# Kernel optimization log

Hardware: AMD Instinct MI355X
Metric: run time of the kernel (lower is better)

The kernel has to match this reference:

```python
import jax, jax.numpy as jnp
import numpy as np

B, S, NGB, NG, DIM = 64, 4096, 13, 48, 3
NCH = [8, 8, 1]
NSHELLS = 8


def setup_inputs() -> dict:
    key = jax.random.key(0)
    ks = jax.random.split(key, 16)
    rng = np.random.default_rng(0)
    # valid row-wise permutations of the N_ngb neighbor slots per group op
    GnnPerms = jnp.asarray(np.argsort(rng.random((NG, NGB)), axis=1), dtype=jnp.int64)
    NNSites = jax.random.randint(ks[0], (NGB, S), 0, S, dtype=jnp.int64)
    SitesToShells = jax.random.randint(ks[1], (S,), 0, NSHELLS, dtype=jnp.int64)
    # block-diagonal (Ng*dim, Ng*dim) cartesian rotation blocks
    blk = rng.normal(size=(NG, DIM, DIM)).astype(np.float32) * 0.5
    gd = np.zeros((NG * DIM, NG * DIM), np.float32)
    for g in range(NG):
        gd[g * DIM:(g + 1) * DIM, g * DIM:(g + 1) * DIM] = blk[g]
    gdiags = jnp.asarray(gd)
    std = 0.2
    return {
        "InStates": jax.random.normal(ks[2], (B, 1, S), jnp.float32),
        "Psi0": jax.random.normal(ks[3], (NCH[0], 1, NGB), jnp.float32) * std,
        "bias0": jax.random.normal(ks[4], (NCH[0], 1), jnp.float32) * std,
        "Psi1": jax.random.normal(ks[5], (NCH[1], NCH[0], NGB), jnp.float32) * std,
        "bias1": jax.random.normal(ks[6], (NCH[1], 1), jnp.float32) * std,
        "Psi2": jax.random.normal(ks[7], (NCH[2], NCH[1], NGB), jnp.float32) * std,
        "bias2": jax.random.normal(ks[8], (NCH[2], 1), jnp.float32) * std,
        "wtVC": jax.random.normal(ks[9], (DIM, NGB), jnp.float32) * std,
        "ShellWeights": jax.random.normal(ks[10], (NSHELLS,), jnp.float32) * std,
        "gdiags": gdiags,
        "GnnPerms": GnnPerms,
        "NNSites": NNSites,
        "SitesToShells": SitesToShells,
    }


def _rearrange(x, NNSites):
    # x: (B, Nch, S) -> (B, Nch*N_ngb, S); subchannel j of channel c holds x[b, c, NNSites[j, s]]
    b, c, s = x.shape
    return x[:, :, NNSites].reshape(b, c * NGB, s)


def _gconv(x, W, b):
    # x: (B, NchIn*N_ngb, S); W: (NchOut, NchIn, N_ngb); b: (NchOut, 1)
    # group-rotated weights: GW[o, g, c*N_ngb+j] = W[o, c, GnnPerms[g, j]]
    GW = _gconv.GW_cache  # set per-call below via closure-free pattern; replaced in reference
    raise NotImplementedError


def reference(InStates, Psi0, bias0, Psi1, bias1, Psi2, bias2, wtVC,
              ShellWeights, gdiags, GnnPerms, NNSites, SitesToShells):
    act = jax.nn.softplus

    def gconv(x, W, b):
        # rotated weights: (NchOut, Ng, NchIn*N_ngb)
        GW = W[:, :, GnnPerms].transpose(0, 2, 1, 3).reshape(W.shape[0], NG, -1)
        h = jnp.einsum('ogk,bks->bogs', GW, x) + b[:, :, None]  # (B, NchOut, Ng, S)
        return act(h).mean(axis=2)                               # group-orbit average

    out = _rearrange(InStates, NNSites)
    for W, b in ((Psi0, bias0), (Psi1, bias1), (Psi2, bias2)):
        out = gconv(out, W, b)                 # (B, NchOut, S)
        out = _rearrange(out, NNSites)         # (B, NchOut*N_ngb, S)
    # vector channel: row g*dim+d of P is wtVC[d, GnnPerms[g]]
    P = wtVC[:, GnnPerms].transpose(1, 0, 2).reshape(NG * DIM, NGB)
    Wvc = gdiags @ P                           # (Ng*dim, N_ngb)
    v = jnp.einsum('kn,bns->bks', Wvc, out)    # (B, Ng*dim, S)
    v = v.reshape(-1, NG, DIM, out.shape[-1]).mean(axis=1)  # (B, dim, S)
    v = v * ShellWeights[SitesToShells]        # per-site shell weighting
    return v.sum(axis=2) / out.shape[-1]       # (B, dim)
```

## Files before the change

### kernel.cpp

```cpp
#include <hip/hip_runtime.h>
#include <hip/hip_bf16.h>

#define BATCH 64
#define SITES 4096
#define NGB 13
#define NGRP 48
#define SDIM 3

typedef __bf16 bf16x8 __attribute__((ext_vector_type(8)));
typedef float  f32x4  __attribute__((ext_vector_type(4)));

#define OFF_AVC  0
#define OFF_U    64
#define OFF_A0   67648
#define OFF_A1   2164800
#define OFF_PART 4261952
#define UW0H 0
#define UW0L 12288
#define UW1H 24576
#define UW1L 73728
#define UW2H 122880
#define UW2L 129024

__device__ __forceinline__ float softplus_f(float h) {
    return fmaxf(h, 0.f) + __logf(1.f + __expf(-fabsf(h)));
}

__global__ __launch_bounds__(256) void precompute_kernel(
    const float* __restrict__ Psi0, const float* __restrict__ Psi1,
    const float* __restrict__ Psi2, const float* __restrict__ wtVC,
    const float* __restrict__ gdiags, const int* __restrict__ perms,
    float* __restrict__ ws)
{
    float*  Avc = ws + OFF_AVC;
    __bf16* U   = (__bf16*)(ws + OFF_U);
    int t = blockIdx.x * 256 + threadIdx.x;
    if (t < 12288) {
        int k = t & 31, row = t >> 5;
        int o = row / NGRP, g = row - o * NGRP;
        float w = (k < NGB) ? Psi0[o * NGB + perms[g * NGB + k]] : 0.f;
        __bf16 hi = (__bf16)w;
        U[UW0H + t] = hi;
        U[UW0L + t] = (__bf16)(w - (float)hi);
    } else if (t < 61440) {
        int u = t - 12288;
        int k = u & 127, row = u >> 7;
        int o = row / NGRP, g = row - o * NGRP;
        float w = 0.f;
        if (k < 104) { int j = k >> 3, c = k & 7;
                       w = Psi1[(o * 8 + c) * NGB + perms[g * NGB + j]]; }
        __bf16 hi = (__bf16)w;
        U[UW1H + u] = hi;
        U[UW1L + u] = (__bf16)(w - (float)hi);
    } else if (t < 67584) {
        int u = t - 61440;
        int k = u & 127, g = u >> 7;
        float w = 0.f;
        if (k < 104) { int j = k >> 3, c = k & 7;
                       w = Psi2[c * NGB + perms[g * NGB + j]]; }
        __bf16 hi = (__bf16)w;
        U[UW2H + u] = hi;
        U[UW2L + u] = (__bf16)(w - (float)hi);
    } else if (t < 67584 + 39 * NGRP) {
        int t2 = t - 67584;
        int g = t2 % NGRP, u = t2 / NGRP;
        int d = u / NGB, n = u % NGB;
        const int row = g * SDIM + d;
        float s = 0.f;
        for (int k = 0; k < NGRP * SDIM; k++) {
            int g2 = k / SDIM, d2 = k - g2 * SDIM;
            float p = wtVC[d2 * NGB + perms[g2 * NGB + n]];
            s = fmaf(gdiags[row * (NGRP * SDIM) + k], p, s);
        }
        atomicAdd(&Avc[u], s * (1.f / 48.f));
    }
}

template<int NCIN, int NCTOT, int CT, int KPAD, int KSTR, int NWAVES, int NWN>
__global__ __launch_bounds__(NWAVES * 64) void layer_mfma(
    const float* __restrict__ prev,
    const __bf16* __restrict__ Wh,
    const __bf16* __restrict__ Wl,
    const float* __restrict__ bias,
    const int*   __restrict__ NN,
    float* __restrict__ out)
{
    constexpr int NTHR   = NWAVES * 64;
    constexpr int K      = NCIN * NGB;
    constexpr int M      = NCTOT * NGRP;
    constexpr int MTILES = M / 16, NTILES = CT / 16;
    constexpr int NWM    = NWAVES / NWN;
    constexpr int MT_W   = MTILES / NWM, NT_W = NTILES / NWN;
    constexpr int KT     = KPAD / 32;

    static_assert(MT_W * 16 == NGRP, "wave covers exactly one o");
    static_assert(NWM * MT_W == MTILES && NWN * NT_W == NTILES, "");
    static_assert((KPAD & 31) == 0 && (KSTR & 7) == 0, "");

    __shared__ __bf16 xh_lds[CT * KSTR];
    __shared__ __bf16 xl_lds[CT * KSTR];

    const int tid  = threadIdx.x;
    const int wave = tid >> 6, lane = tid & 63;
    const int m16  = lane & 15, quad = lane >> 4;

    const int b  = blockIdx.x / (SITES / CT);
    const int s0 = (blockIdx.x % (SITES / CT)) * CT;

    if constexpr (NCIN == 1) {
        for (int site = tid; site < NGB * CT; site += NTHR) {
            int j = site / CT, col = site % CT;
            int nn = NN[j * SITES + s0 + col];
            float v = prev[(size_t)b * SITES + nn];
            __bf16 hi = (__bf16)v;
            xh_lds[col * KSTR + j] = hi;
            xl_lds[col * KSTR + j] = (__bf16)(v - (float)hi);
        }
        for (int e = tid; e < CT * (KPAD - NGB); e += NTHR) {
            int col = e / (KPAD - NGB), p = e % (KPAD - NGB);
            xh_lds[col * KSTR + NGB + p] = (__bf16)0.f;
            xl_lds[col * KSTR + NGB + p] = (__bf16)0.f;
        }
    } else {
        for (int site = tid; site < NGB * CT; site += NTHR) {
            int j = site / CT, col = site % CT;
            int nn = NN[j * SITES + s0 + col];
            const float4* p4 = (const float4*)(prev + ((size_t)(b * SITES + nn)) * 8);
            float4 u0 = p4[0], u1 = p4[1];
            float v[8] = {u0.x, u0.y, u0.z, u0.w, u1.x, u1.y, u1.z, u1.w};
            bf16x8 hv, lv;
#pragma unroll
            for (int c = 0; c < 8; c++) {
                __bf16 hi = (__bf16)v[c];
                hv[c] = hi;
                lv[c] = (__bf16)(v[c] - (float)hi);
            }
            *(bf16x8*)(xh_lds + col * KSTR + j * 8) = hv;
            *(bf16x8*)(xl_lds + col * KSTR + j * 8) = lv;
        }
        const bf16x8 z8 = {};
        for (int e = tid; e < CT * 3; e += NTHR) {
            int col = e % CT, z = e / CT;
            *(bf16x8*)(xh_lds + col * KSTR + 104 + z * 8) = z8;
            *(bf16x8*)(xl_lds + col * KSTR + 104 + z * 8) = z8;
        }
    }
    __syncthreads();

    const int wave_mt0 = (wave / NWN) * MT_W;
    const int wave_nt0 = (wave % NWN) * NT_W;
    const int o_g      = (wave_mt0 * 16) / NGRP;

    f32x4 acc[MT_W][NT_W];
#pragma unroll
    for (int mt = 0; mt < MT_W; mt++)
#pragma unroll
        for (int nt = 0; nt < NT_W; nt++) acc[mt][nt] = (f32x4){0.f, 0.f, 0.f, 0.f};

#pragma unroll
    for (int kt = 0; kt < KT; kt++) {
        const int koff = kt * 32 + quad * 8;
        bf16x8 ah[MT_W], al[MT_W], bh[NT_W], bl[NT_W];
#pragma unroll
        for (int mt = 0; mt < MT_W; mt++) {
            int row = (wave_mt0 + mt) * 16 + m16;
            ah[mt] = *(const bf16x8*)(Wh + (size_t)row * KPAD + koff);
            al[mt] = *(const bf16x8*)(Wl + (size_t)row * KPAD + koff);
        }
#pragma unroll
        for (int nt = 0; nt < NT_W; nt++) {
            int cbase = ((wave_nt0 + nt) * 16 + m16) * KSTR + koff;
            bh[nt] = *(const bf16x8*)(xh_lds + cbase);
            bl[nt] = *(const bf16x8*)(xl_lds + cbase);
        }
#pragma unroll
        for (int mt = 0; mt < MT_W; mt++)
#pragma unroll
            for (int nt = 0; nt < NT_W; nt++) {
                acc[mt][nt] = __builtin_amdgcn_mfma_f32_16x16x32_bf16(
                    ah[mt], bh[nt], acc[mt][nt], 0, 0, 0);
                acc[mt][nt] = __builtin_amdgcn_mfma_f32_16x16x32_bf16(
                    al[mt], bh[nt], acc[mt][nt], 0, 0, 0);
                acc[mt][nt] = __builtin_amdgcn_mfma_f32_16x16x32_bf16(
                    ah[mt], bl[nt], acc[mt][nt], 0, 0, 0);
            }
    }

    const float bo = bias[o_g];
#pragma unroll
    for (int nt = 0; nt < NT_W; nt++) {
        float s = 0.f;
#pragma unroll
        for (int mt = 0; mt < MT_W; mt++)
#pragma unroll
            for (int r = 0; r < 4; r++)
                s += softplus_f(acc[mt][nt][r] + bo);
        s += __shfl_xor(s, 16);
        s += __shfl_xor(s, 32);
        if (quad == 0)
            out[((size_t)(b * SITES + s0 + (wave_nt0 + nt) * 16 + m16)) * NCTOT + o_g]
                = s * (1.f / 48.f);
    }
}

__global__ __launch_bounds__(256) void reduce_a(
    const float* __restrict__ A2, const int* __restrict__ NN,
    const int* __restrict__ s2sh, const float* __restrict__ sw,
    const float* __restrict__ Avc, float* __restrict__ partial)
{
    const int b = blockIdx.x >> 4;
    const int chunk = blockIdx.x & 15;
    const int tid = threadIdx.x;
    const int s = (chunk << 8) + tid;
    const float* a = A2 + (size_t)b * SITES;

    float y0 = 0.f, y1 = 0.f, y2 = 0.f;
#pragma unroll
    for (int n = 0; n < NGB; n++) {
        float v = a[NN[n * SITES + s]];
        y0 = fmaf(Avc[n],           v, y0);
        y1 = fmaf(Avc[NGB + n],     v, y1);
        y2 = fmaf(Avc[2 * NGB + n], v, y2);
    }
    const float wgt = sw[s2sh[s]];
    y0 *= wgt; y1 *= wgt; y2 *= wgt;

    __shared__ float red[3][256];
    red[0][tid] = y0; red[1][tid] = y1; red[2][tid] = y2;
    __syncthreads();
    for (int st = 128; st > 0; st >>= 1) {
        if (tid < st) {
            red[0][tid] += red[0][tid + st];
            red[1][tid] += red[1][tid + st];
            red[2][tid] += red[2][tid + st];
        }
        __syncthreads();
    }
    if (tid < 3) partial[(b * 16 + chunk) * 3 + tid] = red[tid][0];
}

__global__ __launch_bounds__(256) void reduce_b(
    const float* __restrict__ partial, float* __restrict__ out)
{
    int t = threadIdx.x;
    if (t < BATCH * 3) {
        int b = t / 3, d = t - b * 3;
        float s = 0.f;
        for (int c = 0; c < 16; c++) s += partial[(b * 16 + c) * 3 + d];
        out[t] = s * (1.f / (float)SITES);
    }
}

extern "C" void kernel_launch(void* const* d_in, const int* in_sizes, int n_in,
                              void* d_out, int out_size, void* d_ws, size_t ws_size,
                              hipStream_t stream)
{
    const float* InStates = (const float*)d_in[0];
    const float* Psi0     = (const float*)d_in[1];
    const float* bias0    = (const float*)d_in[2];
    const float* Psi1     = (const float*)d_in[3];
    const float* bias1    = (const float*)d_in[4];
    const float* Psi2     = (const float*)d_in[5];
    const float* bias2    = (const float*)d_in[6];
    const float* wtVC     = (const float*)d_in[7];
    const float* ShellW   = (const float*)d_in[8];
    const float* gdiags   = (const float*)d_in[9];
    const int*   GnnPerms = (const int*)d_in[10];
    const int*   NNSites  = (const int*)d_in[11];
    const int*   S2Sh     = (const int*)d_in[12];

    float*  ws   = (float*)d_ws;
    float*  Avc  = ws + OFF_AVC;
    __bf16* U    = (__bf16*)(ws + OFF_U);
    float*  A0   = ws + OFF_A0;
    float*  A1   = ws + OFF_A1;
    float*  A2   = ws + OFF_A0;
    float*  PART = ws + OFF_PART;

    float* out = (float*)d_out;

    hipMemsetAsync(Avc, 0, 39 * sizeof(float), stream);
    precompute_kernel<<<272, 256, 0, stream>>>(Psi0, Psi1, Psi2, wtVC, gdiags,
                                               GnnPerms, ws);

    layer_mfma<1, 8, 64, 32, 40, 8, 1><<<BATCH * (SITES / 64), 512, 0, stream>>>(
        InStates, U + UW0H, U + UW0L, bias0, NNSites, A0);
    layer_mfma<8, 8, 64, 128, 136, 8, 1><<<BATCH * (SITES / 64), 512, 0, stream>>>(
        A0, U + UW1H, U + UW1L, bias1, NNSites, A1);
    layer_mfma<8, 1, 64, 128, 136, 4, 4><<<BATCH * (SITES / 64), 256, 0, stream>>>(
        A1, U + UW2H, U + UW2L, bias2, NNSites, A2);

    reduce_a<<<BATCH * 16, 256, 0, stream>>>(A2, NNSites, S2Sh, ShellW, Avc, PART);
    reduce_b<<<1, 256, 0, stream>>>(PART, out);
}
```

Before: 376.7 us.

## Pipeline neighbor gathers across site tiles and store activations pre-split as bf16 hi/lo

Each layer block now processes four consecutive 64-site tiles, prefetching the next tile's neighbor gather into registers while the current tile's MFMA work runs. Intermediate activations are written as bf16 hi/lo pairs rather than fp32, so the next layer's gather loads them directly without a split-conversion step. Launch bounds request higher occupancy. The changes target gather latency and conversion overhead, at the cost of more registers per thread, extra barriers, and fewer blocks in the grid.

```diff
diff --git a/kernel.cpp b/kernel.cpp
--- a/kernel.cpp
+++ b/kernel.cpp
@@ -12,8 +12,11 @@
 
 #define OFF_AVC  0
 #define OFF_U    64
-#define OFF_A0   67648
-#define OFF_A1   2164800
+#define OFF_AH0  67648
+#define OFF_AL0  1116224
+#define OFF_AH1  2164800
+#define OFF_AL1  3213376
+#define OFF_A2   67648
 #define OFF_PART 4261952
 #define UW0H 0
 #define UW0L 12288
@@ -76,14 +79,19 @@
     }
 }
 
-template<int NCIN, int NCTOT, int CT, int KPAD, int KSTR, int NWAVES, int NWN>
-__global__ __launch_bounds__(NWAVES * 64) void layer_mfma(
-    const float* __restrict__ prev,
+template<int NCIN, int NCTOT, int CT, int KPAD, int KSTR, int NWAVES, int NWN,
+         int P, int SOUT>
+__global__ __launch_bounds__(NWAVES * 64, 4) void layer_pipe(
+    const float*  __restrict__ prevF,
+    const __bf16* __restrict__ prevH,
+    const __bf16* __restrict__ prevL,
     const __bf16* __restrict__ Wh,
     const __bf16* __restrict__ Wl,
-    const float* __restrict__ bias,
-    const int*   __restrict__ NN,
-    float* __restrict__ out)
+    const float*  __restrict__ bias,
+    const int*    __restrict__ NN,
+    float*  __restrict__ outF,
+    __bf16* __restrict__ outH,
+    __bf16* __restrict__ outL)
 {
     constexpr int NTHR   = NWAVES * 64;
     constexpr int K      = NCIN * NGB;
@@ -92,114 +100,158 @@
     constexpr int NWM    = NWAVES / NWN;
     constexpr int MT_W   = MTILES / NWM, NT_W = NTILES / NWN;
     constexpr int KT     = KPAD / 32;
+    constexpr int NSITE  = NGB * CT;
+    constexpr int NSL    = (NSITE + NTHR - 1) / NTHR;
 
     static_assert(MT_W * 16 == NGRP, "wave covers exactly one o");
     static_assert(NWM * MT_W == MTILES && NWN * NT_W == NTILES, "");
     static_assert((KPAD & 31) == 0 && (KSTR & 7) == 0, "");
-
-    __shared__ __bf16 xh_lds[CT * KSTR];
-    __shared__ __bf16 xl_lds[CT * KSTR];
+    static_assert((SITES / CT) % P == 0, "");
+
+    __shared__ __align__(16) __bf16 xh_lds[CT * KSTR];
+    __shared__ __align__(16) __bf16 xl_lds[CT * KSTR];
 
     const int tid  = threadIdx.x;
     const int wave = tid >> 6, lane = tid & 63;
     const int m16  = lane & 15, quad = lane >> 4;
 
-    const int b  = blockIdx.x / (SITES / CT);
-    const int s0 = (blockIdx.x % (SITES / CT)) * CT;
-
-    if constexpr (NCIN == 1) {
-        for (int site = tid; site < NGB * CT; site += NTHR) {
-            int j = site / CT, col = site % CT;
-            int nn = NN[j * SITES + s0 + col];
-            float v = prev[(size_t)b * SITES + nn];
-            __bf16 hi = (__bf16)v;
-            xh_lds[col * KSTR + j] = hi;
-            xl_lds[col * KSTR + j] = (__bf16)(v - (float)hi);
-        }
-        for (int e = tid; e < CT * (KPAD - NGB); e += NTHR) {
-            int col = e / (KPAD - NGB), p = e % (KPAD - NGB);
-            xh_lds[col * KSTR + NGB + p] = (__bf16)0.f;
-            xl_lds[col * KSTR + NGB + p] = (__bf16)0.f;
-        }
-    } else {
-        for (int site = tid; site < NGB * CT; site += NTHR) {
-            int j = site / CT, col = site % CT;
-            int nn = NN[j * SITES + s0 + col];
-            const float4* p4 = (const float4*)(prev + ((size_t)(b * SITES + nn)) * 8);
-            float4 u0 = p4[0], u1 = p4[1];
-            float v[8] = {u0.x, u0.y, u0.z, u0.w, u1.x, u1.y, u1.z, u1.w};
-            bf16x8 hv, lv;
-#pragma unroll
-            for (int c = 0; c < 8; c++) {
-                __bf16 hi = (__bf16)v[c];
-                hv[c] = hi;
-                lv[c] = (__bf16)(v[c] - (float)hi);
-            }
-            *(bf16x8*)(xh_lds + col * KSTR + j * 8) = hv;
-            *(bf16x8*)(xl_lds + col * KSTR + j * 8) = lv;
-        }
+    constexpr int QPB = (SITES / CT) / P;
+    const int b     = blockIdx.x / QPB;
+    const int qq    = blockIdx.x % QPB;
+    const int sbase = qq * (P * CT);
+    const size_t bS = (size_t)b * SITES;
+
+    const int wave_mt0 = (wave / NWN) * MT_W;
+    const int wave_nt0 = (wave % NWN) * NT_W;
+    const int o_g      = (wave_mt0 * 16) / NGRP;
+    const float bo     = bias[o_g];
+
+    if constexpr (NCIN == 8) {
         const bf16x8 z8 = {};
         for (int e = tid; e < CT * 3; e += NTHR) {
             int col = e % CT, z = e / CT;
-            *(bf16x8*)(xh_lds + col * KSTR + 104 + z * 8) = z8;
-            *(bf16x8*)(xl_lds + col * KSTR + 104 + z * 8) = z8;
-        }
-    }
-    __syncthreads();
-
-    const int wave_mt0 = (wave / NWN) * MT_W;
-    const int wave_nt0 = (wave % NWN) * NT_W;
-    const int o_g      = (wave_mt0 * 16) / NGRP;
-
-    f32x4 acc[MT_W][NT_W];
-#pragma unroll
-    for (int mt = 0; mt < MT_W; mt++)
-#pragma unroll
-        for (int nt = 0; nt < NT_W; nt++) acc[mt][nt] = (f32x4){0.f, 0.f, 0.f, 0.f};
-
-#pragma unroll
-    for (int kt = 0; kt < KT; kt++) {
-        const int koff = kt * 32 + quad * 8;
-        bf16x8 ah[MT_W], al[MT_W], bh[NT_W], bl[NT_W];
-#pragma unroll
-        for (int mt = 0; mt < MT_W; mt++) {
-            int row = (wave_mt0 + mt) * 16 + m16;
-            ah[mt] = *(const bf16x8*)(Wh + (size_t)row * KPAD + koff);
-            al[mt] = *(const bf16x8*)(Wl + (size_t)row * KPAD + koff);
-        }
+            *(bf16x8*)(xh_lds + col * KSTR + K + z * 8) = z8;
+            *(bf16x8*)(xl_lds + col * KSTR + K + z * 8) = z8;
+        }
+    } else {
+        for (int e = tid; e < CT * (KPAD - K); e += NTHR) {
+            int col = e % CT, z = e / CT;
+            xh_lds[col * KSTR + K + z] = (__bf16)0.f;
+            xl_lds[col * KSTR + K + z] = (__bf16)0.f;
+        }
+    }
+
+    bf16x8 hreg[NSL], lreg[NSL];
+    float  vreg[NSL];
+
+    auto gather = [&](int pp) {
+        const int s0_ = sbase + pp * CT;
+#pragma unroll
+        for (int i = 0; i < NSL; i++) {
+            int site = tid + i * NTHR;
+            if (site < NSITE) {
+                int j = site / CT, col = site % CT;
+                int nn = NN[j * SITES + s0_ + col];
+                if constexpr (NCIN == 1) {
+                    vreg[i] = prevF[bS + nn];
+                } else {
+                    size_t a8 = (bS + nn) * 8;
+                    hreg[i] = *(const bf16x8*)(prevH + a8);
+                    lreg[i] = *(const bf16x8*)(prevL + a8);
+                }
+            }
+        }
+    };
+
+    auto commit = [&]() {
+#pragma unroll
+        for (int i = 0; i < NSL; i++) {
+            int site = tid + i * NTHR;
+            if (site < NSITE) {
+                int j = site / CT, col = site % CT;
+                if constexpr (NCIN == 1) {
+                    int la = col * KSTR + j;
+                    __bf16 hi = (__bf16)vreg[i];
+                    xh_lds[la] = hi;
+                    xl_lds[la] = (__bf16)(vreg[i] - (float)hi);
+                } else {
+                    int la = col * KSTR + j * 8;
+                    *(bf16x8*)(xh_lds + la) = hreg[i];
+                    *(bf16x8*)(xl_lds + la) = lreg[i];
+                }
+            }
+        }
+    };
+
+    gather(0);
+
+#pragma unroll 1
+    for (int p = 0; p < P; p++) {
+        __syncthreads();
+        commit();
+        __syncthreads();
+        if (p + 1 < P) gather(p + 1);
+
+        const int s0_ = sbase + p * CT;
+        f32x4 acc[MT_W][NT_W];
+#pragma unroll
+        for (int mt = 0; mt < MT_W; mt++)
+#pragma unroll
+            for (int nt = 0; nt < NT_W; nt++)
+                acc[mt][nt] = (f32x4){0.f, 0.f, 0.f, 0.f};
+
+#pragma unroll
+        for (int kt = 0; kt < KT; kt++) {
+            const int koff = kt * 32 + quad * 8;
+            bf16x8 ah[MT_W], al[MT_W], bh[NT_W], bl[NT_W];
+#pragma unroll
+            for (int mt = 0; mt < MT_W; mt++) {
+                int row = (wave_mt0 + mt) * 16 + m16;
+                ah[mt] = *(const bf16x8*)(Wh + (size_t)row * KPAD + koff);
+                al[mt] = *(const bf16x8*)(Wl + (size_t)row * KPAD + koff);
+            }
+#pragma unroll
+            for (int nt = 0; nt < NT_W; nt++) {
+                int cb = ((wave_nt0 + nt) * 16 + m16) * KSTR + koff;
+                bh[nt] = *(const bf16x8*)(xh_lds + cb);
+                bl[nt] = *(const bf16x8*)(xl_lds + cb);
+            }
+#pragma unroll
+            for (int mt = 0; mt < MT_W; mt++)
+#pragma unroll
+                for (int nt = 0; nt < NT_W; nt++) {
+                    acc[mt][nt] = __builtin_amdgcn_mfma_f32_16x16x32_bf16(
+                        ah[mt], bh[nt], acc[mt][nt], 0, 0, 0);
+                    acc[mt][nt] = __builtin_amdgcn_mfma_f32_16x16x32_bf16(
+                        al[mt], bh[nt], acc[mt][nt], 0, 0, 0);
+                    acc[mt][nt] = __builtin_amdgcn_mfma_f32_16x16x32_bf16(
+                        ah[mt], bl[nt], acc[mt][nt], 0, 0, 0);
+                }
+        }
+
 #pragma unroll
         for (int nt = 0; nt < NT_W; nt++) {
-            int cbase = ((wave_nt0 + nt) * 16 + m16) * KSTR + koff;
-            bh[nt] = *(const bf16x8*)(xh_lds + cbase);
-            bl[nt] = *(const bf16x8*)(xl_lds + cbase);
-        }
-#pragma unroll
-        for (int mt = 0; mt < MT_W; mt++)
-#pragma unroll
-            for (int nt = 0; nt < NT_W; nt++) {
-                acc[mt][nt] = __builtin_amdgcn_mfma_f32_16x16x32_bf16(
-                    ah[mt], bh[nt], acc[mt][nt], 0, 0, 0);
-                acc[mt][nt] = __builtin_amdgcn_mfma_f32_16x16x32_bf16(
-                    al[mt], bh[nt], acc[mt][nt], 0, 0, 0);
-                acc[mt][nt] = __builtin_amdgcn_mfma_f32_16x16x32_bf16(
-                    ah[mt], bl[nt], acc[mt][nt], 0, 0, 0);
-            }
-    }
-
-    const float bo = bias[o_g];
-#pragma unroll
-    for (int nt = 0; nt < NT_W; nt++) {
-        float s = 0.f;
-#pragma unroll
-        for (int mt = 0; mt < MT_W; mt++)
-#pragma unroll
-            for (int r = 0; r < 4; r++)
-                s += softplus_f(acc[mt][nt][r] + bo);
-        s += __shfl_xor(s, 16);
-        s += __shfl_xor(s, 32);
-        if (quad == 0)
-            out[((size_t)(b * SITES + s0 + (wave_nt0 + nt) * 16 + m16)) * NCTOT + o_g]
-                = s * (1.f / 48.f);
+            float s = 0.f;
+#pragma unroll
+            for (int mt = 0; mt < MT_W; mt++)
+#pragma unroll
+                for (int r = 0; r < 4; r++)
+                    s += softplus_f(acc[mt][nt][r] + bo);
+            s += __shfl_xor(s, 16);
+            s += __shfl_xor(s, 32);
+            if (quad == 0) {
+                int site = s0_ + (wave_nt0 + nt) * 16 + m16;
+                float val = s * (1.f / 48.f);
+                if constexpr (SOUT) {
+                    size_t idx = (bS + site) * NCTOT + o_g;
+                    __bf16 hi = (__bf16)val;
+                    outH[idx] = hi;
+                    outL[idx] = (__bf16)(val - (float)hi);
+                } else {
+                    outF[bS + site] = val;
+                }
+            }
+        }
     }
 }
 
@@ -272,9 +324,11 @@
     float*  ws   = (float*)d_ws;
     float*  Avc  = ws + OFF_AVC;
     __bf16* U    = (__bf16*)(ws + OFF_U);
-    float*  A0   = ws + OFF_A0;
-    float*  A1   = ws + OFF_A1;
-    float*  A2   = ws + OFF_A0;
+    __bf16* Ah0  = (__bf16*)(ws + OFF_AH0);
+    __bf16* Al0  = (__bf16*)(ws + OFF_AL0);
+    __bf16* Ah1  = (__bf16*)(ws + OFF_AH1);
+    __bf16* Al1  = (__bf16*)(ws + OFF_AL1);
+    float*  A2   = ws + OFF_A2;
     float*  PART = ws + OFF_PART;
 
     float* out = (float*)d_out;
@@ -283,12 +337,15 @@
     precompute_kernel<<<272, 256, 0, stream>>>(Psi0, Psi1, Psi2, wtVC, gdiags,
                                                GnnPerms, ws);
 
-    layer_mfma<1, 8, 64, 32, 40, 8, 1><<<BATCH * (SITES / 64), 512, 0, stream>>>(
-        InStates, U + UW0H, U + UW0L, bias0, NNSites, A0);
-    layer_mfma<8, 8, 64, 128, 136, 8, 1><<<BATCH * (SITES / 64), 512, 0, stream>>>(
-        A0, U + UW1H, U + UW1L, bias1, NNSites, A1);
-    layer_mfma<8, 1, 64, 128, 136, 4, 4><<<BATCH * (SITES / 64), 256, 0, stream>>>(
-        A1, U + UW2H, U + UW2L, bias2, NNSites, A2);
+    layer_pipe<1, 8, 64, 32, 40, 8, 1, 4, 1><<<1024, 512, 0, stream>>>(
+        InStates, nullptr, nullptr, U + UW0H, U + UW0L, bias0, NNSites,
+        nullptr, Ah0, Al0);
+    layer_pipe<8, 8, 64, 128, 136, 8, 1, 4, 1><<<1024, 512, 0, stream>>>(
+        nullptr, Ah0, Al0, U + UW1H, U + UW1L, bias1, NNSites,
+        nullptr, Ah1, Al1);
+    layer_pipe<8, 1, 64, 128, 136, 4, 4, 4, 0><<<1024, 256, 0, stream>>>(
+        nullptr, Ah1, Al1, U + UW2H, U + UW2L, bias2, NNSites,
+        A2, nullptr, nullptr);
 
     reduce_a<<<BATCH * 16, 256, 0, stream>>>(A2, NNSites, S2Sh, ShellW, Avc, PART);
     reduce_b<<<1, 256, 0, stream>>>(PART, out);
```

After: 487.0 us. 29.3% more time.

## Fold biases into GEMM, fuse last layer with reduction via scattered site coefficients

Applied to the files above, without the earlier changes.

Biases are folded into the padded K column of the rotated weights, with a constant-one column added to the activations, so the epilogue no longer adds them. The final gather-and-reduce is transposed: a precompute kernel scatters the vector-channel and shell weights into per-site coefficients C with atomics. The last layer then multiplies its output by C and reduces per block inside one kernel, which removes the A2 round trip and the reduce_a launch. Layer 2 also splits K across two wave halves with an LDS combine, adding two extra barriers; the atomic scatter into C makes the float summation order nondeterministic.

```diff
diff --git a/kernel.cpp b/kernel.cpp
--- a/kernel.cpp
+++ b/kernel.cpp
@@ -14,7 +14,8 @@
 #define OFF_U    64
 #define OFF_A0   67648
 #define OFF_A1   2164800
-#define OFF_PART 4261952
+#define OFF_C    4261952
+#define OFF_PART 4274240
 #define UW0H 0
 #define UW0L 12288
 #define UW1H 24576
@@ -27,8 +28,10 @@
 }
 
 __global__ __launch_bounds__(256) void precompute_kernel(
-    const float* __restrict__ Psi0, const float* __restrict__ Psi1,
-    const float* __restrict__ Psi2, const float* __restrict__ wtVC,
+    const float* __restrict__ Psi0, const float* __restrict__ bias0,
+    const float* __restrict__ Psi1, const float* __restrict__ bias1,
+    const float* __restrict__ Psi2, const float* __restrict__ bias2,
+    const float* __restrict__ wtVC,
     const float* __restrict__ gdiags, const int* __restrict__ perms,
     float* __restrict__ ws)
 {
@@ -38,7 +41,9 @@
     if (t < 12288) {
         int k = t & 31, row = t >> 5;
         int o = row / NGRP, g = row - o * NGRP;
-        float w = (k < NGB) ? Psi0[o * NGB + perms[g * NGB + k]] : 0.f;
+        float w = 0.f;
+        if (k < NGB)       w = Psi0[o * NGB + perms[g * NGB + k]];
+        else if (k == NGB) w = bias0[o];
         __bf16 hi = (__bf16)w;
         U[UW0H + t] = hi;
         U[UW0L + t] = (__bf16)(w - (float)hi);
@@ -49,6 +54,7 @@
         float w = 0.f;
         if (k < 104) { int j = k >> 3, c = k & 7;
                        w = Psi1[(o * 8 + c) * NGB + perms[g * NGB + j]]; }
+        else if (k == 104) w = bias1[o];
         __bf16 hi = (__bf16)w;
         U[UW1H + u] = hi;
         U[UW1L + u] = (__bf16)(w - (float)hi);
@@ -58,6 +64,7 @@
         float w = 0.f;
         if (k < 104) { int j = k >> 3, c = k & 7;
                        w = Psi2[c * NGB + perms[g * NGB + j]]; }
+        else if (k == 104) w = bias2[0];
         __bf16 hi = (__bf16)w;
         U[UW2H + u] = hi;
         U[UW2L + u] = (__bf16)(w - (float)hi);
@@ -76,12 +83,27 @@
     }
 }
 
+__global__ __launch_bounds__(256) void precompute_C(
+    const int* __restrict__ NN, const int* __restrict__ s2sh,
+    const float* __restrict__ sw, const float* __restrict__ ws_avc,
+    float* __restrict__ C)
+{
+    int e = blockIdx.x * 256 + threadIdx.x;
+    if (e < NGB * SITES) {
+        int n = e >> 12, s = e & (SITES - 1);
+        int t = NN[n * SITES + s];
+        float w = sw[s2sh[s]];
+        atomicAdd(&C[t],            ws_avc[n] * w);
+        atomicAdd(&C[SITES + t],    ws_avc[NGB + n] * w);
+        atomicAdd(&C[2 * SITES + t], ws_avc[2 * NGB + n] * w);
+    }
+}
+
 template<int NCIN, int NCTOT, int CT, int KPAD, int KSTR, int NWAVES, int NWN>
 __global__ __launch_bounds__(NWAVES * 64) void layer_mfma(
     const float* __restrict__ prev,
     const __bf16* __restrict__ Wh,
     const __bf16* __restrict__ Wl,
-    const float* __restrict__ bias,
     const int*   __restrict__ NN,
     float* __restrict__ out)
 {
@@ -97,8 +119,8 @@
     static_assert(NWM * MT_W == MTILES && NWN * NT_W == NTILES, "");
     static_assert((KPAD & 31) == 0 && (KSTR & 7) == 0, "");
 
-    __shared__ __bf16 xh_lds[CT * KSTR];
-    __shared__ __bf16 xl_lds[CT * KSTR];
+    __shared__ __align__(16) __bf16 xh_lds[CT * KSTR];
+    __shared__ __align__(16) __bf16 xl_lds[CT * KSTR];
 
     const int tid  = threadIdx.x;
     const int wave = tid >> 6, lane = tid & 63;
@@ -116,10 +138,10 @@
             xh_lds[col * KSTR + j] = hi;
             xl_lds[col * KSTR + j] = (__bf16)(v - (float)hi);
         }
-        for (int e = tid; e < CT * (KPAD - NGB); e += NTHR) {
-            int col = e / (KPAD - NGB), p = e % (KPAD - NGB);
-            xh_lds[col * KSTR + NGB + p] = (__bf16)0.f;
-            xl_lds[col * KSTR + NGB + p] = (__bf16)0.f;
+        for (int e = tid; e < CT * (KPAD - K); e += NTHR) {
+            int col = e / (KPAD - K), p = e % (KPAD - K);
+            xh_lds[col * KSTR + K + p] = (p == 0) ? (__bf16)1.f : (__bf16)0.f;
+            xl_lds[col * KSTR + K + p] = (__bf16)0.f;
         }
     } else {
         for (int site = tid; site < NGB * CT; site += NTHR) {
@@ -138,11 +160,13 @@
             *(bf16x8*)(xh_lds + col * KSTR + j * 8) = hv;
             *(bf16x8*)(xl_lds + col * KSTR + j * 8) = lv;
         }
-        const bf16x8 z8 = {};
+        bf16x8 z8 = {};
+        bf16x8 one8 = {};
+        one8[0] = (__bf16)1.f;
         for (int e = tid; e < CT * 3; e += NTHR) {
             int col = e % CT, z = e / CT;
-            *(bf16x8*)(xh_lds + col * KSTR + 104 + z * 8) = z8;
-            *(bf16x8*)(xl_lds + col * KSTR + 104 + z * 8) = z8;
+            *(bf16x8*)(xh_lds + col * KSTR + K + z * 8) = (z == 0) ? one8 : z8;
+            *(bf16x8*)(xl_lds + col * KSTR + K + z * 8) = z8;
         }
     }
     __syncthreads();
@@ -186,7 +210,6 @@
             }
     }
 
-    const float bo = bias[o_g];
 #pragma unroll
     for (int nt = 0; nt < NT_W; nt++) {
         float s = 0.f;
@@ -194,7 +217,7 @@
         for (int mt = 0; mt < MT_W; mt++)
 #pragma unroll
             for (int r = 0; r < 4; r++)
-                s += softplus_f(acc[mt][nt][r] + bo);
+                s += softplus_f(acc[mt][nt][r]);
         s += __shfl_xor(s, 16);
         s += __shfl_xor(s, 32);
         if (quad == 0)
@@ -203,50 +226,133 @@
     }
 }
 
-__global__ __launch_bounds__(256) void reduce_a(
-    const float* __restrict__ A2, const int* __restrict__ NN,
-    const int* __restrict__ s2sh, const float* __restrict__ sw,
-    const float* __restrict__ Avc, float* __restrict__ partial)
-{
-    const int b = blockIdx.x >> 4;
-    const int chunk = blockIdx.x & 15;
-    const int tid = threadIdx.x;
-    const int s = (chunk << 8) + tid;
-    const float* a = A2 + (size_t)b * SITES;
-
-    float y0 = 0.f, y1 = 0.f, y2 = 0.f;
-#pragma unroll
-    for (int n = 0; n < NGB; n++) {
-        float v = a[NN[n * SITES + s]];
-        y0 = fmaf(Avc[n],           v, y0);
-        y1 = fmaf(Avc[NGB + n],     v, y1);
-        y2 = fmaf(Avc[2 * NGB + n], v, y2);
-    }
-    const float wgt = sw[s2sh[s]];
-    y0 *= wgt; y1 *= wgt; y2 *= wgt;
-
-    __shared__ float red[3][256];
-    red[0][tid] = y0; red[1][tid] = y1; red[2][tid] = y2;
+__global__ __launch_bounds__(512) void layer2_fused(
+    const float* __restrict__ prev,
+    const __bf16* __restrict__ Wh,
+    const __bf16* __restrict__ Wl,
+    const int* __restrict__ NN,
+    const float* __restrict__ C,
+    float* __restrict__ part)
+{
+    constexpr int CT = 64, KPAD = 128, KSTR = 136, K = 104;
+
+    __shared__ __align__(16) __bf16 xh_lds[CT * KSTR];
+    __shared__ __align__(16) __bf16 xl_lds[CT * KSTR];
+    __shared__ float wsum[4][3];
+
+    const int tid  = threadIdx.x;
+    const int wave = tid >> 6, lane = tid & 63;
+    const int m16  = lane & 15, quad = lane >> 4;
+
+    const int b     = blockIdx.x >> 6;
+    const int chunk = blockIdx.x & 63;
+    const int s0    = chunk * CT;
+    const size_t bS = (size_t)b * SITES;
+
+    for (int site = tid; site < NGB * CT; site += 512) {
+        int j = site / CT, col = site % CT;
+        int nn = NN[j * SITES + s0 + col];
+        const float4* p4 = (const float4*)(prev + (bS + nn) * 8);
+        float4 u0 = p4[0], u1 = p4[1];
+        float v[8] = {u0.x, u0.y, u0.z, u0.w, u1.x, u1.y, u1.z, u1.w};
+        bf16x8 hv, lv;
+#pragma unroll
+        for (int c = 0; c < 8; c++) {
+            __bf16 hi = (__bf16)v[c];
+            hv[c] = hi;
+            lv[c] = (__bf16)(v[c] - (float)hi);
+        }
+        *(bf16x8*)(xh_lds + col * KSTR + j * 8) = hv;
+        *(bf16x8*)(xl_lds + col * KSTR + j * 8) = lv;
+    }
+    {
+        bf16x8 z8 = {};
+        bf16x8 one8 = {};
+        one8[0] = (__bf16)1.f;
+        for (int e = tid; e < CT * 3; e += 512) {
+            int col = e % CT, z = e / CT;
+            *(bf16x8*)(xh_lds + col * KSTR + K + z * 8) = (z == 0) ? one8 : z8;
+            *(bf16x8*)(xl_lds + col * KSTR + K + z * 8) = z8;
+        }
+    }
     __syncthreads();
-    for (int st = 128; st > 0; st >>= 1) {
-        if (tid < st) {
-            red[0][tid] += red[0][tid + st];
-            red[1][tid] += red[1][tid + st];
-            red[2][tid] += red[2][tid + st];
-        }
-        __syncthreads();
-    }
-    if (tid < 3) partial[(b * 16 + chunk) * 3 + tid] = red[tid][0];
+
+    const int nt = wave & 3, kh = wave >> 2;
+
+    f32x4 acc[3];
+#pragma unroll
+    for (int mt = 0; mt < 3; mt++) acc[mt] = (f32x4){0.f, 0.f, 0.f, 0.f};
+
+#pragma unroll
+    for (int kk = 0; kk < 2; kk++) {
+        const int koff = (kh * 2 + kk) * 32 + quad * 8;
+        bf16x8 ah[3], al[3];
+#pragma unroll
+        for (int mt = 0; mt < 3; mt++) {
+            int row = mt * 16 + m16;
+            ah[mt] = *(const bf16x8*)(Wh + (size_t)row * KPAD + koff);
+            al[mt] = *(const bf16x8*)(Wl + (size_t)row * KPAD + koff);
+        }
+        int cbase = (nt * 16 + m16) * KSTR + koff;
+        bf16x8 bh = *(const bf16x8*)(xh_lds + cbase);
+        bf16x8 bl = *(const bf16x8*)(xl_lds + cbase);
+#pragma unroll
+        for (int mt = 0; mt < 3; mt++) {
+            acc[mt] = __builtin_amdgcn_mfma_f32_16x16x32_bf16(ah[mt], bh, acc[mt], 0, 0, 0);
+            acc[mt] = __builtin_amdgcn_mfma_f32_16x16x32_bf16(al[mt], bh, acc[mt], 0, 0, 0);
+            acc[mt] = __builtin_amdgcn_mfma_f32_16x16x32_bf16(ah[mt], bl, acc[mt], 0, 0, 0);
+        }
+    }
+    __syncthreads();
+
+    float* hpart = (float*)xh_lds;
+    if (kh == 1) {
+#pragma unroll
+        for (int mt = 0; mt < 3; mt++)
+#pragma unroll
+            for (int r = 0; r < 4; r++)
+                hpart[nt * 768 + (mt * 16 + quad * 4 + r) * 16 + m16] = acc[mt][r];
+    }
+    __syncthreads();
+
+    if (kh == 0) {
+        float s = 0.f;
+#pragma unroll
+        for (int mt = 0; mt < 3; mt++)
+#pragma unroll
+            for (int r = 0; r < 4; r++)
+                s += softplus_f(acc[mt][r] +
+                                hpart[nt * 768 + (mt * 16 + quad * 4 + r) * 16 + m16]);
+        s += __shfl_xor(s, 16);
+        s += __shfl_xor(s, 32);
+        float a2 = s * (1.f / 48.f);
+        int site = s0 + nt * 16 + m16;
+        float y0 = a2 * C[site];
+        float y1 = a2 * C[SITES + site];
+        float y2 = a2 * C[2 * SITES + site];
+#pragma unroll
+        for (int d = 1; d <= 8; d <<= 1) {
+            y0 += __shfl_xor(y0, d);
+            y1 += __shfl_xor(y1, d);
+            y2 += __shfl_xor(y2, d);
+        }
+        if (lane == 0) { wsum[nt][0] = y0; wsum[nt][1] = y1; wsum[nt][2] = y2; }
+    }
+    __syncthreads();
+    if (tid < 3) {
+        float s = wsum[0][tid] + wsum[1][tid] + wsum[2][tid] + wsum[3][tid];
+        part[blockIdx.x * 3 + tid] = s;
+    }
 }
 
 __global__ __launch_bounds__(256) void reduce_b(
-    const float* __restrict__ partial, float* __restrict__ out)
+    const float* __restrict__ part, float* __restrict__ out)
 {
     int t = threadIdx.x;
     if (t < BATCH * 3) {
         int b = t / 3, d = t - b * 3;
         float s = 0.f;
-        for (int c = 0; c < 16; c++) s += partial[(b * 16 + c) * 3 + d];
+        for (int c = 0; c < 64; c++) s += part[(b * 64 + c) * 3 + d];
         out[t] = s * (1.f / (float)SITES);
     }
 }
@@ -274,22 +380,25 @@
     __bf16* U    = (__bf16*)(ws + OFF_U);
     float*  A0   = ws + OFF_A0;
     float*  A1   = ws + OFF_A1;
-    float*  A2   = ws + OFF_A0;
+    float*  C    = ws + OFF_C;
     float*  PART = ws + OFF_PART;
 
     float* out = (float*)d_out;
 
     hipMemsetAsync(Avc, 0, 39 * sizeof(float), stream);
-    precompute_kernel<<<272, 256, 0, stream>>>(Psi0, Psi1, Psi2, wtVC, gdiags,
+    hipMemsetAsync(C, 0, 3 * SITES * sizeof(float), stream);
+
+    precompute_kernel<<<272, 256, 0, stream>>>(Psi0, bias0, Psi1, bias1,
+                                               Psi2, bias2, wtVC, gdiags,
                                                GnnPerms, ws);
+    precompute_C<<<208, 256, 0, stream>>>(NNSites, S2Sh, ShellW, Avc, C);
 
     layer_mfma<1, 8, 64, 32, 40, 8, 1><<<BATCH * (SITES / 64), 512, 0, stream>>>(
-        InStates, U + UW0H, U + UW0L, bias0, NNSites, A0);
+        InStates, U + UW0H, U + UW0L, NNSites, A0);
     layer_mfma<8, 8, 64, 128, 136, 8, 1><<<BATCH * (SITES / 64), 512, 0, stream>>>(
-        A0, U + UW1H, U + UW1L, bias1, NNSites, A1);
-    layer_mfma<8, 1, 64, 128, 136, 4, 4><<<BATCH * (SITES / 64), 256, 0, stream>>>(
-        A1, U + UW2H, U + UW2L, bias2, NNSites, A2);
-
-    reduce_a<<<BATCH * 16, 256, 0, stream>>>(A2, NNSites, S2Sh, ShellW, Avc, PART);
+        A0, U + UW1H, U + UW1L, NNSites, A1);
+    layer2_fused<<<BATCH * 64, 512, 0, stream>>>(
+        A1, U + UW2H, U + UW2L, NNSites, C, PART);
+
     reduce_b<<<1, 256, 0, stream>>>(PART, out);
 }
```

After: 395.5 us. 1.05x slower.
